# Performance work log

Hardware: AMD Instinct MI355X
Metric: run time of the kernel (lower is better)

The kernel has to match this reference:

```python
import jax, jax.numpy as jnp
import numpy as np

B, M, QT, KVT, H = 2, 16, 1024, 4096, 128


def setup_inputs() -> dict:
    key = jax.random.key(0)
    kq, kk = jax.random.split(key)
    q = jax.random.normal(kq, (B, M, QT, H), dtype=jnp.float32)
    k = jax.random.normal(kk, (B, M, KVT, H), dtype=jnp.float32)
    return {"q": q, "k": k}


def reference(q, k):
    # Original: broadcast multiply q[B,M,QT,1,H] * k[B,M,1,KVT,H], sum over H.
    # Mathematically identical to a batched QK^T contraction over head dim.
    # score: [B, M, QT, KVT]
    return jnp.einsum('bmqh,bmkh->bmqk', q, k)
```

## Files before the change

kernel.cpp:

```cpp
#include <hip/hip_runtime.h>


#define QT   1024
#define KVT  4096
#define HD   128
#define NXCD 8

using bf16x8 = __attribute__((ext_vector_type(8))) __bf16;
using bf16x4 = __attribute__((ext_vector_type(4))) __bf16;
using f32x16 = __attribute__((ext_vector_type(16))) float;

__global__ __launch_bounds__(256, 4)
void QKBmm_74062416052397_kernel(const float* __restrict__ q,
                                 const float* __restrict__ k,
                                 float* __restrict__ out) {
    __shared__ __bf16 As[32 * 64];
    __shared__ __bf16 Bs[256 * 64];

    const int t = threadIdx.x;

    const unsigned lin = blockIdx.x;
    const unsigned swz = (lin & (NXCD - 1)) * (16384u / NXCD) + (lin >> 3);
    const int nt_ = swz & 15;
    const int mt  = (swz >> 4) & 31;
    const int bm  = swz >> 9;
    const int m0  = mt * 32;
    const int n0  = nt_ * 256;

    const float4* __restrict__ Q4 =
        reinterpret_cast<const float4*>(q + ((size_t)bm * QT  + m0) * HD);
    const float4* __restrict__ K4 =
        reinterpret_cast<const float4*>(k + ((size_t)bm * KVT + n0) * HD);

    const int lane = t & 63;
    const int wid  = t >> 6;
    const int wn   = wid * 64;
    const int l31  = lane & 31;
    const int kh   = (lane >> 5) * 8;

    f32x16 acc[2] = {};

#pragma unroll
    for (int h = 0; h < 2; ++h) {
        if (h) __syncthreads();

        {
            float4 v0, v1;
            int f0 = t,       r0 = f0 >> 4, c0 = f0 & 15;
            int f1 = 256 + t, r1 = f1 >> 4, c1 = f1 & 15;
            v0 = Q4[r0 * 32 + h * 16 + c0];
            v1 = Q4[r1 * 32 + h * 16 + c1];
            int e0 = (r0 * 64 + c0 * 4) ^ ((r0 & 7) << 3);
            int e1 = (r1 * 64 + c1 * 4) ^ ((r1 & 7) << 3);
            *reinterpret_cast<bf16x4*>(&As[e0]) =
                bf16x4{ (__bf16)v0.x, (__bf16)v0.y, (__bf16)v0.z, (__bf16)v0.w };
            *reinterpret_cast<bf16x4*>(&As[e1]) =
                bf16x4{ (__bf16)v1.x, (__bf16)v1.y, (__bf16)v1.z, (__bf16)v1.w };
        }
#pragma unroll
        for (int b4 = 0; b4 < 4; ++b4) {
            float4 v[4];
#pragma unroll
            for (int j = 0; j < 4; ++j) {
                int f = (b4 * 4 + j) * 256 + t, row = f >> 4, c4 = f & 15;
                v[j] = K4[row * 32 + h * 16 + c4];
            }
#pragma unroll
            for (int j = 0; j < 4; ++j) {
                int f = (b4 * 4 + j) * 256 + t, row = f >> 4, c4 = f & 15;
                int e = (row * 64 + c4 * 4) ^ ((row & 7) << 3);
                *reinterpret_cast<bf16x4*>(&Bs[e]) =
                    bf16x4{ (__bf16)v[j].x, (__bf16)v[j].y,
                            (__bf16)v[j].z, (__bf16)v[j].w };
            }
        }
        __syncthreads();

#pragma unroll
        for (int ks = 0; ks < 4; ++ks) {
            const int kcol = ks * 16 + kh;
            int ra = l31;
            int ea = (ra * 64 + kcol) ^ ((ra & 7) << 3);
            bf16x8 af = *reinterpret_cast<const bf16x8*>(&As[ea]);
#pragma unroll
            for (int ni = 0; ni < 2; ++ni) {
                int rb = wn + ni * 32 + l31;
                int eb = (rb * 64 + kcol) ^ ((rb & 7) << 3);
                bf16x8 bfr = *reinterpret_cast<const bf16x8*>(&Bs[eb]);
                acc[ni] = __builtin_amdgcn_mfma_f32_32x32x16_bf16(
                    af, bfr, acc[ni], 0, 0, 0);
            }
        }
    }

    float* __restrict__ Cp = out + (size_t)bm * QT * KVT;
#pragma unroll
    for (int ni = 0; ni < 2; ++ni) {
#pragma unroll
        for (int r = 0; r < 16; ++r) {
            int row = m0 + (r & 3) + 8 * (r >> 2) + 4 * (lane >> 5);
            float* rp = Cp + (size_t)row * KVT + n0 + wn + ni * 32 + l31;
            __builtin_nontemporal_store(acc[ni][r], rp);
        }
    }
}

extern "C" void kernel_launch(void* const* d_in, const int* in_sizes, int n_in,
                              void* d_out, int out_size, void* d_ws, size_t ws_size,
                              hipStream_t stream) {
    const float* q = (const float*)d_in[0];
    const float* k = (const float*)d_in[1];
    float* out = (float*)d_out;

    QKBmm_74062416052397_kernel<<<dim3(16384), dim3(256), 0, stream>>>(q, k, out);
}
```

Before: 140.1 us.

## Switch to 64x128 block tiles and prefetch second K-half during compute

Changes the per-block output tile from 32x256 to 64x128, arranging the four waves as a 2x2 grid so both Q and K tiles are reused across waves. The global loads for the second half of the head dimension are issued before the first half's MFMA loop so their latency overlaps with compute. Loaded data per block drops from 288 to 192 rows of head dimension. The extra prefetch registers raise VGPR pressure and may reduce occupancy.

```diff
diff --git a/kernel.cpp b/kernel.cpp
--- a/kernel.cpp
+++ b/kernel.cpp
@@ -14,18 +14,18 @@
 void QKBmm_74062416052397_kernel(const float* __restrict__ q,
                                  const float* __restrict__ k,
                                  float* __restrict__ out) {
-    __shared__ __bf16 As[32 * 64];
-    __shared__ __bf16 Bs[256 * 64];
+    __shared__ __bf16 As[64 * 64];
+    __shared__ __bf16 Bs[128 * 64];
 
     const int t = threadIdx.x;
 
     const unsigned lin = blockIdx.x;
     const unsigned swz = (lin & (NXCD - 1)) * (16384u / NXCD) + (lin >> 3);
-    const int nt_ = swz & 15;
-    const int mt  = (swz >> 4) & 31;
+    const int nt_ = swz & 31;
+    const int mt  = (swz >> 5) & 15;
     const int bm  = swz >> 9;
-    const int m0  = mt * 32;
-    const int n0  = nt_ * 256;
+    const int m0  = mt * 64;
+    const int n0  = nt_ * 128;
 
     const float4* __restrict__ Q4 =
         reinterpret_cast<const float4*>(q + ((size_t)bm * QT  + m0) * HD);
@@ -34,62 +34,107 @@
 
     const int lane = t & 63;
     const int wid  = t >> 6;
-    const int wn   = wid * 64;
+    const int wm   = (wid >> 1) * 32;
+    const int wn   = (wid & 1) * 64;
     const int l31  = lane & 31;
     const int kh   = (lane >> 5) * 8;
 
     f32x16 acc[2] = {};
 
+
+    float4 qa[4], kb[8];
 #pragma unroll
-    for (int h = 0; h < 2; ++h) {
-        if (h) __syncthreads();
-
-        {
-            float4 v0, v1;
-            int f0 = t,       r0 = f0 >> 4, c0 = f0 & 15;
-            int f1 = 256 + t, r1 = f1 >> 4, c1 = f1 & 15;
-            v0 = Q4[r0 * 32 + h * 16 + c0];
-            v1 = Q4[r1 * 32 + h * 16 + c1];
-            int e0 = (r0 * 64 + c0 * 4) ^ ((r0 & 7) << 3);
-            int e1 = (r1 * 64 + c1 * 4) ^ ((r1 & 7) << 3);
-            *reinterpret_cast<bf16x4*>(&As[e0]) =
-                bf16x4{ (__bf16)v0.x, (__bf16)v0.y, (__bf16)v0.z, (__bf16)v0.w };
-            *reinterpret_cast<bf16x4*>(&As[e1]) =
-                bf16x4{ (__bf16)v1.x, (__bf16)v1.y, (__bf16)v1.z, (__bf16)v1.w };
-        }
+    for (int it = 0; it < 4; ++it) {
+        int f = it * 256 + t, r = f >> 4, c = f & 15;
+        qa[it] = Q4[r * 32 + c];
+    }
 #pragma unroll
-        for (int b4 = 0; b4 < 4; ++b4) {
-            float4 v[4];
-#pragma unroll
-            for (int j = 0; j < 4; ++j) {
-                int f = (b4 * 4 + j) * 256 + t, row = f >> 4, c4 = f & 15;
-                v[j] = K4[row * 32 + h * 16 + c4];
-            }
-#pragma unroll
-            for (int j = 0; j < 4; ++j) {
-                int f = (b4 * 4 + j) * 256 + t, row = f >> 4, c4 = f & 15;
-                int e = (row * 64 + c4 * 4) ^ ((row & 7) << 3);
-                *reinterpret_cast<bf16x4*>(&Bs[e]) =
-                    bf16x4{ (__bf16)v[j].x, (__bf16)v[j].y,
-                            (__bf16)v[j].z, (__bf16)v[j].w };
-            }
-        }
-        __syncthreads();
+    for (int it = 0; it < 8; ++it) {
+        int f = it * 256 + t, r = f >> 4, c = f & 15;
+        kb[it] = K4[r * 32 + c];
+    }
 
 #pragma unroll
-        for (int ks = 0; ks < 4; ++ks) {
-            const int kcol = ks * 16 + kh;
-            int ra = l31;
-            int ea = (ra * 64 + kcol) ^ ((ra & 7) << 3);
-            bf16x8 af = *reinterpret_cast<const bf16x8*>(&As[ea]);
+    for (int it = 0; it < 4; ++it) {
+        int f = it * 256 + t, r = f >> 4, c = f & 15;
+        int e = (r * 64 + c * 4) ^ ((r & 7) << 3);
+        *reinterpret_cast<bf16x4*>(&As[e]) =
+            bf16x4{ (__bf16)qa[it].x, (__bf16)qa[it].y,
+                    (__bf16)qa[it].z, (__bf16)qa[it].w };
+    }
 #pragma unroll
-            for (int ni = 0; ni < 2; ++ni) {
-                int rb = wn + ni * 32 + l31;
-                int eb = (rb * 64 + kcol) ^ ((rb & 7) << 3);
-                bf16x8 bfr = *reinterpret_cast<const bf16x8*>(&Bs[eb]);
-                acc[ni] = __builtin_amdgcn_mfma_f32_32x32x16_bf16(
-                    af, bfr, acc[ni], 0, 0, 0);
-            }
+    for (int it = 0; it < 8; ++it) {
+        int f = it * 256 + t, r = f >> 4, c = f & 15;
+        int e = (r * 64 + c * 4) ^ ((r & 7) << 3);
+        *reinterpret_cast<bf16x4*>(&Bs[e]) =
+            bf16x4{ (__bf16)kb[it].x, (__bf16)kb[it].y,
+                    (__bf16)kb[it].z, (__bf16)kb[it].w };
+    }
+
+    float4 qa1[4], kb1[8];
+#pragma unroll
+    for (int it = 0; it < 4; ++it) {
+        int f = it * 256 + t, r = f >> 4, c = f & 15;
+        qa1[it] = Q4[r * 32 + 16 + c];
+    }
+#pragma unroll
+    for (int it = 0; it < 8; ++it) {
+        int f = it * 256 + t, r = f >> 4, c = f & 15;
+        kb1[it] = K4[r * 32 + 16 + c];
+    }
+
+    __syncthreads();
+
+#pragma unroll
+    for (int ks = 0; ks < 4; ++ks) {
+        const int kcol = ks * 16 + kh;
+        int ra = wm + l31;
+        int ea = (ra * 64 + kcol) ^ ((ra & 7) << 3);
+        bf16x8 af = *reinterpret_cast<const bf16x8*>(&As[ea]);
+#pragma unroll
+        for (int ni = 0; ni < 2; ++ni) {
+            int rb = wn + ni * 32 + l31;
+            int eb = (rb * 64 + kcol) ^ ((rb & 7) << 3);
+            bf16x8 bfr = *reinterpret_cast<const bf16x8*>(&Bs[eb]);
+            acc[ni] = __builtin_amdgcn_mfma_f32_32x32x16_bf16(
+                af, bfr, acc[ni], 0, 0, 0);
+        }
+    }
+
+    __syncthreads();
+
+#pragma unroll
+    for (int it = 0; it < 4; ++it) {
+        int f = it * 256 + t, r = f >> 4, c = f & 15;
+        int e = (r * 64 + c * 4) ^ ((r & 7) << 3);
+        *reinterpret_cast<bf16x4*>(&As[e]) =
+            bf16x4{ (__bf16)qa1[it].x, (__bf16)qa1[it].y,
+                    (__bf16)qa1[it].z, (__bf16)qa1[it].w };
+    }
+#pragma unroll
+    for (int it = 0; it < 8; ++it) {
+        int f = it * 256 + t, r = f >> 4, c = f & 15;
+        int e = (r * 64 + c * 4) ^ ((r & 7) << 3);
+        *reinterpret_cast<bf16x4*>(&Bs[e]) =
+            bf16x4{ (__bf16)kb1[it].x, (__bf16)kb1[it].y,
+                    (__bf16)kb1[it].z, (__bf16)kb1[it].w };
+    }
+
+    __syncthreads();
+
+#pragma unroll
+    for (int ks = 0; ks < 4; ++ks) {
+        const int kcol = ks * 16 + kh;
+        int ra = wm + l31;
+        int ea = (ra * 64 + kcol) ^ ((ra & 7) << 3);
+        bf16x8 af = *reinterpret_cast<const bf16x8*>(&As[ea]);
+#pragma unroll
+        for (int ni = 0; ni < 2; ++ni) {
+            int rb = wn + ni * 32 + l31;
+            int eb = (rb * 64 + kcol) ^ ((rb & 7) << 3);
+            bf16x8 bfr = *reinterpret_cast<const bf16x8*>(&Bs[eb]);
+            acc[ni] = __builtin_amdgcn_mfma_f32_32x32x16_bf16(
+                af, bfr, acc[ni], 0, 0, 0);
         }
     }
 
@@ -98,7 +143,7 @@
     for (int ni = 0; ni < 2; ++ni) {
 #pragma unroll
         for (int r = 0; r < 16; ++r) {
-            int row = m0 + (r & 3) + 8 * (r >> 2) + 4 * (lane >> 5);
+            int row = m0 + wm + (r & 3) + 8 * (r >> 2) + 4 * (lane >> 5);
             float* rp = Cp + (size_t)row * KVT + n0 + wn + ni * 32 + l31;
             __builtin_nontemporal_store(acc[ni][r], rp);
         }
```

After: 117.6 us. 1.19x faster.
